# Optimization experiments

Measured on AMD Instinct MI355X. Metric: run time of the kernel, lower is better.

Reference implementation:

```python
import jax, jax.numpy as jnp
import numpy as np

N_NODES = 50000
N_EDGES = 800000
IN_DIM = 128
HID = 128
BN_EPS = 1e-5


def setup_inputs() -> dict:
    key = jax.random.key(0)
    ks = jax.random.split(key, 8)
    x = jax.random.normal(ks[0], (N_NODES, IN_DIM), dtype=jnp.float32)
    edge_index = jax.random.randint(ks[1], (2, N_EDGES), 0, N_NODES, dtype=jnp.int64)
    s1 = 1.0 / np.sqrt(IN_DIM)
    s2 = 1.0 / np.sqrt(HID)
    return {
        'x': x,
        'edge_index': edge_index,
        'w1_0': jax.random.normal(ks[2], (IN_DIM, HID), dtype=jnp.float32) * s1,
        'b1_0': jnp.zeros((HID,), dtype=jnp.float32),
        'w2_0': jax.random.normal(ks[3], (HID, HID), dtype=jnp.float32) * s2,
        'b2_0': jnp.zeros((HID,), dtype=jnp.float32),
        'g_0': jnp.ones((HID,), dtype=jnp.float32),
        'be_0': jnp.zeros((HID,), dtype=jnp.float32),
        'w1_1': jax.random.normal(ks[4], (HID, HID), dtype=jnp.float32) * s2,
        'b1_1': jnp.zeros((HID,), dtype=jnp.float32),
        'w2_1': jax.random.normal(ks[5], (HID, HID), dtype=jnp.float32) * s2,
        'b2_1': jnp.zeros((HID,), dtype=jnp.float32),
        'g_1': jnp.ones((HID,), dtype=jnp.float32),
        'be_1': jnp.zeros((HID,), dtype=jnp.float32),
    }


def _gin_layer(h, src, dst, w1, b1, w2, b2, g, be):
    # GINConv with eps=0: MLP(h_i + sum_{j->i} h_j); scatter-add over targets
    agg = jax.ops.segment_sum(h[src], dst, num_segments=N_NODES)
    z = h + agg
    z = jax.nn.relu(z @ w1 + b1) @ w2 + b2
    # BatchNorm1d (training mode: batch stats over nodes, biased variance)
    mu = jnp.mean(z, axis=0)
    var = jnp.mean(jnp.square(z - mu), axis=0)
    z = (z - mu) * jax.lax.rsqrt(var + BN_EPS) * g + be
    return jax.nn.relu(z)


def reference(x, edge_index, w1_0, b1_0, w2_0, b2_0, g_0, be_0,
              w1_1, b1_1, w2_1, b2_1, g_1, be_1):
    src, dst = edge_index[0], edge_index[1]
    h = _gin_layer(x, src, dst, w1_0, b1_0, w2_0, b2_0, g_0, be_0)
    # dropout p=0.0 -> no-op between layers
    h = _gin_layer(h, src, dst, w1_1, b1_1, w2_1, b2_1, g_1, be_1)
    return h
```

## Files before the change

kernel.cpp:

```cpp
#include <hip/hip_runtime.h>
#include <hip/hip_bf16.h>

#define HID 128
#define LDA 136
#define BINSH 4
#define BINSZ 16
#define NBH 3136
#define EPB 4096
#define ECAP 768
#define CAP 64

typedef __attribute__((ext_vector_type(8))) short frag8;
typedef __attribute__((ext_vector_type(4))) float f32x4;

__device__ inline float bf2f(unsigned short u) {
    return __uint_as_float(((unsigned int)u) << 16);
}
__device__ inline unsigned short f2bf(float f) {
    __hip_bfloat16 h = __float2bfloat16(f);
    return __builtin_bit_cast(unsigned short, h);
}
__device__ inline float4 u4tof4(ushort4 u) {
    return make_float4(bf2f(u.x), bf2f(u.y), bf2f(u.z), bf2f(u.w));
}
__device__ inline ushort4 f4tou4(float4 f) {
    ushort4 u; u.x = f2bf(f.x); u.y = f2bf(f.y); u.z = f2bf(f.z); u.w = f2bf(f.w);
    return u;
}
__device__ inline void unpack8(uint4 u, float* f) {
    const unsigned* w = (const unsigned*)&u;
    #pragma unroll
    for (int j = 0; j < 4; j++) {
        f[2 * j]     = __uint_as_float(w[j] << 16);
        f[2 * j + 1] = __uint_as_float(w[j] & 0xffff0000u);
    }
}

__global__ __launch_bounds__(256) void hist_k(
    const int* __restrict__ dst, int* __restrict__ Hst,
    const float* __restrict__ x, unsigned short* __restrict__ B0,
    const float* __restrict__ w0, const float* __restrict__ w1,
    const float* __restrict__ w2, const float* __restrict__ w3,
    unsigned short* __restrict__ wt,
    int n_edges, long total4, int hb, int vb)
{
    __shared__ int hist[NBH];
    const int bid = blockIdx.x;
    const int t = threadIdx.x;

    if (bid < hb) {
        for (int j = t; j < NBH; j += 256) hist[j] = 0;
        __syncthreads();
        const int base = bid * EPB;
        const int cnt = min(EPB, n_edges - base);
        for (int i = t; i < cnt; i += 256)
            atomicAdd(&hist[dst[base + i] >> BINSH], 1);
        __syncthreads();
        for (int j = t; j < NBH; j += 256)
            Hst[(size_t)bid * NBH + j] = hist[j];
    } else if (bid < hb + vb) {
        long i = (long)(bid - hb) * 256 + t;
        if (i < total4) {
            float4 v = ((const float4*)x)[i];
            ((ushort4*)B0)[i] = f4tou4(v);
        }
    } else {
        int w_id = bid - hb - vb;
        const float* w = (w_id == 0) ? w0 : (w_id == 1) ? w1 : (w_id == 2) ? w2 : w3;
        unsigned short* o = wt + (size_t)w_id * 128 * 128;
        for (int i = 0; i < 64; i++) {
            int idx = t + i * 256;
            o[(idx & 127) * 128 + (idx >> 7)] = f2bf(w[idx]);
        }
    }
}

__global__ __launch_bounds__(256) void colscan_k(
    int* __restrict__ Hst, int* __restrict__ colsum, int nblk)
{
    int b = blockIdx.x * 256 + threadIdx.x;
    if (b >= NBH) return;
    int run = 0;
    int i = 0;
    for (; i + 4 <= nblk; i += 4) {
        int* p0 = &Hst[(size_t)(i + 0) * NBH + b];
        int* p1 = &Hst[(size_t)(i + 1) * NBH + b];
        int* p2 = &Hst[(size_t)(i + 2) * NBH + b];
        int* p3 = &Hst[(size_t)(i + 3) * NBH + b];
        int v0 = *p0, v1 = *p1, v2 = *p2, v3 = *p3;
        *p0 = run; run += v0;
        *p1 = run; run += v1;
        *p2 = run; run += v2;
        *p3 = run; run += v3;
    }
    for (; i < nblk; i++) {
        int v = Hst[(size_t)i * NBH + b];
        Hst[(size_t)i * NBH + b] = run;
        run += v;
    }
    colsum[b] = run;
}

__global__ __launch_bounds__(1024) void binscan_k(
    const int* __restrict__ colsum, int* __restrict__ binStart,
    float* __restrict__ S0, float* __restrict__ S1)
{
    __shared__ int s[NBH];
    __shared__ int c[1024];
    const int t = threadIdx.x;
    if (t < 256) S0[t] = 0.f;
    else if (t < 512) S1[t - 256] = 0.f;
    for (int j = t; j < NBH; j += 1024) s[j] = colsum[j];
    __syncthreads();

    int l0 = 0, l1 = 0, l2 = 0, l3 = 0, sum = 0;
    if (t < NBH / 4) {
        int b = t * 4;
        l0 = s[b]; l1 = s[b + 1]; l2 = s[b + 2]; l3 = s[b + 3];
        sum = l0 + l1 + l2 + l3;
    }
    c[t] = sum;
    __syncthreads();
    for (int off = 1; off < 1024; off <<= 1) {
        int v = (t >= off) ? c[t - off] : 0;
        __syncthreads();
        c[t] += v;
        __syncthreads();
    }
    if (t < NBH / 4) {
        int ex = c[t] - sum;
        int b = t * 4;
        binStart[b] = ex;
        binStart[b + 1] = ex + l0;
        binStart[b + 2] = ex + l0 + l1;
        binStart[b + 3] = ex + l0 + l1 + l2;
    }
}

__global__ __launch_bounds__(256) void place_k(
    const int* __restrict__ src, const int* __restrict__ dst,
    const int* __restrict__ Hst, const int* __restrict__ binStart,
    int* __restrict__ binned, int n_edges)
{
    __shared__ int hist[NBH];
    const int bid = blockIdx.x;
    const int t = threadIdx.x;
    for (int j = t; j < NBH; j += 256) hist[j] = 0;
    __syncthreads();
    const int base = bid * EPB;
    const int cnt = min(EPB, n_edges - base);
    const int* Hrow = Hst + (size_t)bid * NBH;
    for (int i = t; i < cnt; i += 256) {
        int e = base + i;
        int d = dst[e];
        int bin = d >> BINSH;
        int r = atomicAdd(&hist[bin], 1);
        int pos = binStart[bin] + Hrow[bin] + r;
        binned[pos] = (src[e] << BINSH) | (d & (BINSZ - 1));
    }
}

template<bool BN>
__global__ __launch_bounds__(512) void gather_k(
    const unsigned short* __restrict__ h, unsigned short* __restrict__ z,
    const int* __restrict__ binStart, const int* __restrict__ colsum,
    const int* __restrict__ binned,
    const float* __restrict__ S, const float* __restrict__ g,
    const float* __restrict__ be, float inv_n, int n)
{
    __shared__ int Ls[ECAP];
    __shared__ int cnt16[BINSZ];
    __shared__ int perNode[BINSZ * CAP];
    __shared__ float lscS[BN ? 128 : 1], lshS[BN ? 128 : 1];

    const int t = threadIdx.x;
    const int bin = blockIdx.x;
    const int v0 = bin << BINSH;

    if (t < BINSZ) cnt16[t] = 0;
    if (BN && t < 128) {
        float mu = S[t] * inv_n;
        float var = fmaf(-mu, mu, S[128 + t] * inv_n);
        float s = g[t] * rsqrtf(var + 1e-5f);
        lscS[t] = s;
        lshS[t] = fmaf(-mu, s, be[t]);
    }
    const int base = binStart[bin];
    const int total = min(colsum[bin], ECAP);
    for (int j = t; j < total; j += 512) Ls[j] = binned[base + j];
    __syncthreads();

    for (int j = t; j < total; j += 512) {
        int pa = Ls[j];
        int node = pa & (BINSZ - 1);
        int p = atomicAdd(&cnt16[node], 1);
        if (p < CAP) perNode[node * CAP + p] = pa >> BINSH;
    }
    __syncthreads();

    const int vl = t >> 5;
    const int v = v0 + vl;
    if (v >= n) return;
    const int lane = t & 31;
    const int fs = (lane & 15) * 8;
    const int par = lane >> 4;

    float sc[8], sh[8];
    if (BN) {
        #pragma unroll
        for (int j = 0; j < 8; j++) { sc[j] = lscS[fs + j]; sh[j] = lshS[fs + j]; }
    }

    float acc[8];
    #pragma unroll
    for (int j = 0; j < 8; j++) acc[j] = 0.f;

    if (par == 0) {
        uint4 u = *(const uint4*)(h + (size_t)v * HID + fs);
        float f[8];
        unpack8(u, f);
        #pragma unroll
        for (int j = 0; j < 8; j++) {
            float xv = f[j];
            if (BN) xv = fmaxf(fmaf(xv, sc[j], sh[j]), 0.f);
            acc[j] = xv;
        }
    }

    const int* bucket = perNode + vl * CAP;
    int deg = min(cnt16[vl], CAP);

    int i = par;
    for (; i + 6 < deg; i += 8) {
        int s0 = bucket[i], s1 = bucket[i + 2];
        int s2 = bucket[i + 4], s3 = bucket[i + 6];
        uint4 u0 = *(const uint4*)(h + (size_t)s0 * HID + fs);
        uint4 u1 = *(const uint4*)(h + (size_t)s1 * HID + fs);
        uint4 u2 = *(const uint4*)(h + (size_t)s2 * HID + fs);
        uint4 u3 = *(const uint4*)(h + (size_t)s3 * HID + fs);
        float f0[8], f1[8], f2[8], f3[8];
        unpack8(u0, f0); unpack8(u1, f1); unpack8(u2, f2); unpack8(u3, f3);
        if (BN) {
            #pragma unroll
            for (int j = 0; j < 8; j++) {
                f0[j] = fmaxf(fmaf(f0[j], sc[j], sh[j]), 0.f);
                f1[j] = fmaxf(fmaf(f1[j], sc[j], sh[j]), 0.f);
                f2[j] = fmaxf(fmaf(f2[j], sc[j], sh[j]), 0.f);
                f3[j] = fmaxf(fmaf(f3[j], sc[j], sh[j]), 0.f);
            }
        }
        #pragma unroll
        for (int j = 0; j < 8; j++)
            acc[j] += (f0[j] + f1[j]) + (f2[j] + f3[j]);
    }
    for (; i < deg; i += 2) {
        uint4 u = *(const uint4*)(h + (size_t)bucket[i] * HID + fs);
        float f[8];
        unpack8(u, f);
        if (BN) {
            #pragma unroll
            for (int j = 0; j < 8; j++)
                f[j] = fmaxf(fmaf(f[j], sc[j], sh[j]), 0.f);
        }
        #pragma unroll
        for (int j = 0; j < 8; j++) acc[j] += f[j];
    }

    #pragma unroll
    for (int j = 0; j < 8; j++) acc[j] += __shfl_xor(acc[j], 16);

    if (par == 0) {
        unsigned o[4];
        #pragma unroll
        for (int j = 0; j < 4; j++)
            o[j] = (unsigned)f2bf(acc[2 * j]) |
                   ((unsigned)f2bf(acc[2 * j + 1]) << 16);
        *(uint4*)(z + (size_t)v * HID + fs) = make_uint4(o[0], o[1], o[2], o[3]);
    }
}

__global__ __launch_bounds__(256) void mlp_k(
    unsigned short* __restrict__ Z,
    const unsigned short* __restrict__ W1t, const float* __restrict__ b1,
    const unsigned short* __restrict__ W2t, const float* __restrict__ b2,
    float* __restrict__ S, int n_rows)
{
    __shared__ unsigned short Hs[128 * LDA];
    __shared__ float red[1024];

    const int t = threadIdx.x;
    const int row0 = blockIdx.x * 128;
    const int wave = t >> 6;
    const int lane = t & 63;
    const int l15  = lane & 15;
    const int quad = lane >> 4;

    const int r0 = row0 + wave * 32 + l15;
    const int r1 = r0 + 16;
    const int rs0 = (r0 < n_rows) ? r0 : 0;
    const int rs1 = (r1 < n_rows) ? r1 : 0;
    frag8 a0[4], a1[4];
    #pragma unroll
    for (int kk = 0; kk < 4; kk++) {
        a0[kk] = *(const frag8*)(Z + (size_t)rs0 * HID + kk * 32 + quad * 8);
        a1[kk] = *(const frag8*)(Z + (size_t)rs1 * HID + kk * 32 + quad * 8);
    }

    f32x4 acc[2][8];
    #pragma unroll
    for (int tr = 0; tr < 2; tr++)
        #pragma unroll
        for (int tc = 0; tc < 8; tc++)
            acc[tr][tc] = (f32x4){0.f, 0.f, 0.f, 0.f};

    #pragma unroll
    for (int kk = 0; kk < 4; kk++) {
        int ko = kk * 32 + quad * 8;
        #pragma unroll
        for (int tc = 0; tc < 8; tc++) {
            frag8 b = *(const frag8*)(W1t + (size_t)(tc * 16 + l15) * HID + ko);
            acc[0][tc] = __builtin_amdgcn_mfma_f32_16x16x32_bf16(a0[kk], b, acc[0][tc], 0, 0, 0);
            acc[1][tc] = __builtin_amdgcn_mfma_f32_16x16x32_bf16(a1[kk], b, acc[1][tc], 0, 0, 0);
        }
    }

    const int wrow = wave * 32;
    #pragma unroll
    for (int tc = 0; tc < 8; tc++) {
        const int col = tc * 16 + l15;
        const float bc = b1[col];
        #pragma unroll
        for (int tr = 0; tr < 2; tr++)
            #pragma unroll
            for (int r = 0; r < 4; r++) {
                int lrow = wrow + tr * 16 + quad * 4 + r;
                Hs[lrow * LDA + col] = f2bf(fmaxf(acc[tr][tc][r] + bc, 0.f));
            }
    }
    __syncthreads();

    #pragma unroll
    for (int kk = 0; kk < 4; kk++) {
        a0[kk] = *(const frag8*)(Hs + (wave * 32 + l15) * LDA + kk * 32 + quad * 8);
        a1[kk] = *(const frag8*)(Hs + (wave * 32 + 16 + l15) * LDA + kk * 32 + quad * 8);
    }
    #pragma unroll
    for (int tr = 0; tr < 2; tr++)
        #pragma unroll
        for (int tc = 0; tc < 8; tc++)
            acc[tr][tc] = (f32x4){0.f, 0.f, 0.f, 0.f};

    #pragma unroll
    for (int kk = 0; kk < 4; kk++) {
        int ko = kk * 32 + quad * 8;
        #pragma unroll
        for (int tc = 0; tc < 8; tc++) {
            frag8 b = *(const frag8*)(W2t + (size_t)(tc * 16 + l15) * HID + ko);
            acc[0][tc] = __builtin_amdgcn_mfma_f32_16x16x32_bf16(a0[kk], b, acc[0][tc], 0, 0, 0);
            acc[1][tc] = __builtin_amdgcn_mfma_f32_16x16x32_bf16(a1[kk], b, acc[1][tc], 0, 0, 0);
        }
    }

    #pragma unroll
    for (int tc = 0; tc < 8; tc++) {
        const int col = tc * 16 + l15;
        const float bc = b2[col];
        float s = 0.f, sq = 0.f;
        #pragma unroll
        for (int tr = 0; tr < 2; tr++)
            #pragma unroll
            for (int r = 0; r < 4; r++) {
                int grow = row0 + wrow + tr * 16 + quad * 4 + r;
                float o = acc[tr][tc][r] + bc;
                if (grow < n_rows) {
                    s += o; sq = fmaf(o, o, sq);
                    Z[(size_t)grow * HID + col] = f2bf(o);
                }
            }
        s  += __shfl_xor(s, 16);  s  += __shfl_xor(s, 32);
        sq += __shfl_xor(sq, 16); sq += __shfl_xor(sq, 32);
        if (lane < 16) {
            red[wave * 128 + col] = s;
            red[512 + wave * 128 + col] = sq;
        }
    }
    __syncthreads();
    {
        int which = t >> 7, c = t & 127;
        const float* rp = red + which * 512;
        atomicAdd(&S[which * 128 + c],
                  rp[c] + rp[128 + c] + rp[256 + c] + rp[384 + c]);
    }
}

__global__ __launch_bounds__(256) void bn_apply_f32_k(
    const unsigned short* __restrict__ z, const float* __restrict__ S,
    const float* __restrict__ g, const float* __restrict__ be,
    float* __restrict__ out, float inv_n, long total4)
{
    __shared__ float lsc[128], lsh[128];
    int t = threadIdx.x;
    if (t < 128) {
        float mu = S[t] * inv_n;
        float var = fmaf(-mu, mu, S[128 + t] * inv_n);
        float s = g[t] * rsqrtf(var + 1e-5f);
        lsc[t] = s;
        lsh[t] = fmaf(-mu, s, be[t]);
    }
    __syncthreads();

    long i = blockIdx.x * 256L + t;
    if (i >= total4) return;
    float4 v = u4tof4(((const ushort4*)z)[i]);
    int c0 = ((int)(i & 31)) * 4;
    v.x = fmaxf(fmaf(v.x, lsc[c0 + 0], lsh[c0 + 0]), 0.0f);
    v.y = fmaxf(fmaf(v.y, lsc[c0 + 1], lsh[c0 + 1]), 0.0f);
    v.z = fmaxf(fmaf(v.z, lsc[c0 + 2], lsh[c0 + 2]), 0.0f);
    v.w = fmaxf(fmaf(v.w, lsc[c0 + 3], lsh[c0 + 3]), 0.0f);
    ((float4*)out)[i] = v;
}

extern "C" void kernel_launch(void* const* d_in, const int* in_sizes, int n_in,
                              void* d_out, int out_size, void* d_ws, size_t ws_size,
                              hipStream_t stream)
{
    const float* x    = (const float*)d_in[0];
    const int*   ei   = (const int*)d_in[1];
    const float* w1_0 = (const float*)d_in[2];
    const float* b1_0 = (const float*)d_in[3];
    const float* w2_0 = (const float*)d_in[4];
    const float* b2_0 = (const float*)d_in[5];
    const float* g_0  = (const float*)d_in[6];
    const float* be_0 = (const float*)d_in[7];
    const float* w1_1 = (const float*)d_in[8];
    const float* b1_1 = (const float*)d_in[9];
    const float* w2_1 = (const float*)d_in[10];
    const float* b2_1 = (const float*)d_in[11];
    const float* g_1  = (const float*)d_in[12];
    const float* be_1 = (const float*)d_in[13];
    float* OUT = (float*)d_out;

    const int n       = in_sizes[0] / HID;
    const int n_edges = in_sizes[1] / 2;
    const int* src = ei;
    const int* dst = ei + n_edges;
    const float inv_n = 1.0f / (float)n;
    const int n_bins = (n + BINSZ - 1) / BINSZ;

    char* p = (char*)d_ws;
    unsigned short* B0 = (unsigned short*)p;  p += (size_t)n * HID * sizeof(short);
    unsigned short* B1 = (unsigned short*)p;  p += (size_t)n * HID * sizeof(short);
    unsigned short* Wt = (unsigned short*)p;  p += (size_t)4 * 128 * 128 * sizeof(short);
    const int nblk = (n_edges + EPB - 1) / EPB;
    int*   Hst      = (int*)p;   p += (size_t)nblk * NBH * sizeof(int);
    int*   colsum   = (int*)p;   p += NBH * sizeof(int);
    int*   binStart = (int*)p;   p += NBH * sizeof(int);
    float* S0       = (float*)p; p += 256 * sizeof(float);
    float* S1       = (float*)p; p += 256 * sizeof(float);
    int*   binned   = (int*)p;   p += (size_t)n_edges * sizeof(int);

    dim3 blk(256);
    const long total4 = (long)n * (HID / 4);
    const int vb = (int)((total4 + 255) / 256);

    hist_k<<<nblk + vb + 4, blk, 0, stream>>>(
        dst, Hst, x, B0, w1_0, w2_0, w1_1, w2_1, Wt, n_edges, total4, nblk, vb);
    colscan_k<<<(NBH + 255) / 256, blk, 0, stream>>>(Hst, colsum, nblk);
    binscan_k<<<1, dim3(1024), 0, stream>>>(colsum, binStart, S0, S1);
    place_k<<<nblk, blk, 0, stream>>>(src, dst, Hst, binStart, binned, n_edges);

    gather_k<false><<<n_bins, dim3(512), 0, stream>>>(
        B0, B1, binStart, colsum, binned, nullptr, nullptr, nullptr, inv_n, n);
    mlp_k<<<(n + 127) / 128, blk, 0, stream>>>(B1, Wt, b1_0, Wt + 16384, b2_0, S0, n);

    gather_k<true><<<n_bins, dim3(512), 0, stream>>>(
        B1, B0, binStart, colsum, binned, S0, g_0, be_0, inv_n, n);
    mlp_k<<<(n + 127) / 128, blk, 0, stream>>>(B0, Wt + 2 * 16384, b1_1,
                                               Wt + 3 * 16384, b2_1, S1, n);
    bn_apply_f32_k<<<vb, blk, 0, stream>>>(B0, S1, g_1, be_1, OUT, inv_n, total4);
}
```

Before: 282.5 us.

## Fuse neighbor gather into MLP kernel with 128-node bins and separate BN pass

```diff
diff --git a/kernel.cpp b/kernel.cpp
--- a/kernel.cpp
+++ b/kernel.cpp
@@ -7,7 +7,6 @@
 #define BINSZ 16
 #define NBH 3136
 #define EPB 4096
-#define ECAP 768
 #define CAP 64
 
 typedef __attribute__((ext_vector_type(8))) short frag8;
@@ -156,171 +155,119 @@
         int bin = d >> BINSH;
         int r = atomicAdd(&hist[bin], 1);
         int pos = binStart[bin] + Hrow[bin] + r;
-        binned[pos] = (src[e] << BINSH) | (d & (BINSZ - 1));
-    }
-}
-
-template<bool BN>
-__global__ __launch_bounds__(512) void gather_k(
-    const unsigned short* __restrict__ h, unsigned short* __restrict__ z,
-    const int* __restrict__ binStart, const int* __restrict__ colsum,
-    const int* __restrict__ binned,
-    const float* __restrict__ S, const float* __restrict__ g,
-    const float* __restrict__ be, float inv_n, int n)
-{
-    __shared__ int Ls[ECAP];
-    __shared__ int cnt16[BINSZ];
-    __shared__ int perNode[BINSZ * CAP];
-    __shared__ float lscS[BN ? 128 : 1], lshS[BN ? 128 : 1];
+        binned[pos] = (src[e] << 7) | (d & 127);
+    }
+}
+
+__device__ inline void gather_row(const unsigned short* __restrict__ Hin,
+                                  int gr, int n, const int* __restrict__ bp,
+                                  int deg, int fo, frag8* out)
+{
+    float acc[4][8];
+    if (gr < n) {
+        #pragma unroll
+        for (int kk = 0; kk < 4; kk++) {
+            uint4 u = *(const uint4*)(Hin + (size_t)gr * HID + fo + kk * 32);
+            unpack8(u, acc[kk]);
+        }
+    } else {
+        #pragma unroll
+        for (int kk = 0; kk < 4; kk++)
+            #pragma unroll
+            for (int j = 0; j < 8; j++) acc[kk][j] = 0.f;
+    }
+    int i = 0;
+    for (; i + 2 <= deg; i += 2) {
+        int sA = bp[i], sB = bp[i + 1];
+        uint4 uA[4], uB[4];
+        #pragma unroll
+        for (int kk = 0; kk < 4; kk++) {
+            uA[kk] = *(const uint4*)(Hin + (size_t)sA * HID + fo + kk * 32);
+            uB[kk] = *(const uint4*)(Hin + (size_t)sB * HID + fo + kk * 32);
+        }
+        #pragma unroll
+        for (int kk = 0; kk < 4; kk++) {
+            float fA[8], fB[8];
+            unpack8(uA[kk], fA);
+            unpack8(uB[kk], fB);
+            #pragma unroll
+            for (int j = 0; j < 8; j++) acc[kk][j] += fA[j] + fB[j];
+        }
+    }
+    if (i < deg) {
+        int sA = bp[i];
+        #pragma unroll
+        for (int kk = 0; kk < 4; kk++) {
+            uint4 u = *(const uint4*)(Hin + (size_t)sA * HID + fo + kk * 32);
+            float fA[8];
+            unpack8(u, fA);
+            #pragma unroll
+            for (int j = 0; j < 8; j++) acc[kk][j] += fA[j];
+        }
+    }
+    #pragma unroll
+    for (int kk = 0; kk < 4; kk++) {
+        frag8 f;
+        #pragma unroll
+        for (int j = 0; j < 8; j++) f[j] = (short)f2bf(acc[kk][j]);
+        out[kk] = f;
+    }
+}
+
+__global__ __launch_bounds__(256) void gmlp_k(
+    const unsigned short* __restrict__ Hin, unsigned short* __restrict__ Zout,
+    const int* __restrict__ binStart, const int* __restrict__ binned,
+    const float* __restrict__ b1v, const unsigned short* __restrict__ W1t,
+    const float* __restrict__ b2v, const unsigned short* __restrict__ W2t,
+    float* __restrict__ SOut, int n, int n_edges)
+{
+    __shared__ __align__(16) unsigned char uS[128 * LDA * 2];
+    int* perNode = (int*)uS;
+    unsigned short* Hs = (unsigned short*)uS;
+    __shared__ int cnt[128];
+    __shared__ float red[1024];
 
     const int t = threadIdx.x;
-    const int bin = blockIdx.x;
-    const int v0 = bin << BINSH;
-
-    if (t < BINSZ) cnt16[t] = 0;
-    if (BN && t < 128) {
-        float mu = S[t] * inv_n;
-        float var = fmaf(-mu, mu, S[128 + t] * inv_n);
-        float s = g[t] * rsqrtf(var + 1e-5f);
-        lscS[t] = s;
-        lshS[t] = fmaf(-mu, s, be[t]);
-    }
-    const int base = binStart[bin];
-    const int total = min(colsum[bin], ECAP);
-    for (int j = t; j < total; j += 512) Ls[j] = binned[base + j];
-    __syncthreads();
-
-    for (int j = t; j < total; j += 512) {
-        int pa = Ls[j];
-        int node = pa & (BINSZ - 1);
-        int p = atomicAdd(&cnt16[node], 1);
-        if (p < CAP) perNode[node * CAP + p] = pa >> BINSH;
-    }
-    __syncthreads();
-
-    const int vl = t >> 5;
-    const int v = v0 + vl;
-    if (v >= n) return;
-    const int lane = t & 31;
-    const int fs = (lane & 15) * 8;
-    const int par = lane >> 4;
-
-    float sc[8], sh[8];
-    if (BN) {
-        #pragma unroll
-        for (int j = 0; j < 8; j++) { sc[j] = lscS[fs + j]; sh[j] = lshS[fs + j]; }
-    }
-
-    float acc[8];
-    #pragma unroll
-    for (int j = 0; j < 8; j++) acc[j] = 0.f;
-
-    if (par == 0) {
-        uint4 u = *(const uint4*)(h + (size_t)v * HID + fs);
-        float f[8];
-        unpack8(u, f);
-        #pragma unroll
-        for (int j = 0; j < 8; j++) {
-            float xv = f[j];
-            if (BN) xv = fmaxf(fmaf(xv, sc[j], sh[j]), 0.f);
-            acc[j] = xv;
-        }
-    }
-
-    const int* bucket = perNode + vl * CAP;
-    int deg = min(cnt16[vl], CAP);
-
-    int i = par;
-    for (; i + 6 < deg; i += 8) {
-        int s0 = bucket[i], s1 = bucket[i + 2];
-        int s2 = bucket[i + 4], s3 = bucket[i + 6];
-        uint4 u0 = *(const uint4*)(h + (size_t)s0 * HID + fs);
-        uint4 u1 = *(const uint4*)(h + (size_t)s1 * HID + fs);
-        uint4 u2 = *(const uint4*)(h + (size_t)s2 * HID + fs);
-        uint4 u3 = *(const uint4*)(h + (size_t)s3 * HID + fs);
-        float f0[8], f1[8], f2[8], f3[8];
-        unpack8(u0, f0); unpack8(u1, f1); unpack8(u2, f2); unpack8(u3, f3);
-        if (BN) {
-            #pragma unroll
-            for (int j = 0; j < 8; j++) {
-                f0[j] = fmaxf(fmaf(f0[j], sc[j], sh[j]), 0.f);
-                f1[j] = fmaxf(fmaf(f1[j], sc[j], sh[j]), 0.f);
-                f2[j] = fmaxf(fmaf(f2[j], sc[j], sh[j]), 0.f);
-                f3[j] = fmaxf(fmaf(f3[j], sc[j], sh[j]), 0.f);
-            }
-        }
-        #pragma unroll
-        for (int j = 0; j < 8; j++)
-            acc[j] += (f0[j] + f1[j]) + (f2[j] + f3[j]);
-    }
-    for (; i < deg; i += 2) {
-        uint4 u = *(const uint4*)(h + (size_t)bucket[i] * HID + fs);
-        float f[8];
-        unpack8(u, f);
-        if (BN) {
-            #pragma unroll
-            for (int j = 0; j < 8; j++)
-                f[j] = fmaxf(fmaf(f[j], sc[j], sh[j]), 0.f);
-        }
-        #pragma unroll
-        for (int j = 0; j < 8; j++) acc[j] += f[j];
-    }
-
-    #pragma unroll
-    for (int j = 0; j < 8; j++) acc[j] += __shfl_xor(acc[j], 16);
-
-    if (par == 0) {
-        unsigned o[4];
-        #pragma unroll
-        for (int j = 0; j < 4; j++)
-            o[j] = (unsigned)f2bf(acc[2 * j]) |
-                   ((unsigned)f2bf(acc[2 * j + 1]) << 16);
-        *(uint4*)(z + (size_t)v * HID + fs) = make_uint4(o[0], o[1], o[2], o[3]);
-    }
-}
-
-__global__ __launch_bounds__(256) void mlp_k(
-    unsigned short* __restrict__ Z,
-    const unsigned short* __restrict__ W1t, const float* __restrict__ b1,
-    const unsigned short* __restrict__ W2t, const float* __restrict__ b2,
-    float* __restrict__ S, int n_rows)
-{
-    __shared__ unsigned short Hs[128 * LDA];
-    __shared__ float red[1024];
-
-    const int t = threadIdx.x;
-    const int row0 = blockIdx.x * 128;
-    const int wave = t >> 6;
-    const int lane = t & 63;
-    const int l15  = lane & 15;
-    const int quad = lane >> 4;
-
-    const int r0 = row0 + wave * 32 + l15;
-    const int r1 = r0 + 16;
-    const int rs0 = (r0 < n_rows) ? r0 : 0;
-    const int rs1 = (r1 < n_rows) ? r1 : 0;
+    const int v0 = blockIdx.x * 128;
+
+    if (t < 128) cnt[t] = 0;
+    __syncthreads();
+
+    const int gbin = blockIdx.x * 8;
+    const int jstart = binStart[gbin];
+    const int jend = binStart[gbin + 8];
+    for (int j = jstart + t; j < jend; j += 256) {
+        int e = binned[j];
+        int node = e & 127;
+        int p = atomicAdd(&cnt[node], 1);
+        if (p < CAP) perNode[node * CAP + p] = e >> 7;
+    }
+    __syncthreads();
+
+    const int wave = t >> 6, lane = t & 63, l15 = lane & 15, quad = lane >> 4;
+    const int lr0 = wave * 32 + l15, lr1 = lr0 + 16;
+    const int fo = quad * 8;
+
     frag8 a0[4], a1[4];
+    gather_row(Hin, v0 + lr0, n, perNode + lr0 * CAP, min(cnt[lr0], CAP), fo, a0);
+    gather_row(Hin, v0 + lr1, n, perNode + lr1 * CAP, min(cnt[lr1], CAP), fo, a1);
+    __syncthreads();
+
+    f32x4 macc[2][8];
+    #pragma unroll
+    for (int tr = 0; tr < 2; tr++)
+        #pragma unroll
+        for (int tc = 0; tc < 8; tc++)
+            macc[tr][tc] = (f32x4){0.f, 0.f, 0.f, 0.f};
+
     #pragma unroll
     for (int kk = 0; kk < 4; kk++) {
-        a0[kk] = *(const frag8*)(Z + (size_t)rs0 * HID + kk * 32 + quad * 8);
-        a1[kk] = *(const frag8*)(Z + (size_t)rs1 * HID + kk * 32 + quad * 8);
-    }
-
-    f32x4 acc[2][8];
-    #pragma unroll
-    for (int tr = 0; tr < 2; tr++)
-        #pragma unroll
-        for (int tc = 0; tc < 8; tc++)
-            acc[tr][tc] = (f32x4){0.f, 0.f, 0.f, 0.f};
-
-    #pragma unroll
-    for (int kk = 0; kk < 4; kk++) {
-        int ko = kk * 32 + quad * 8;
+        int ko = fo + kk * 32;
         #pragma unroll
         for (int tc = 0; tc < 8; tc++) {
             frag8 b = *(const frag8*)(W1t + (size_t)(tc * 16 + l15) * HID + ko);
-            acc[0][tc] = __builtin_amdgcn_mfma_f32_16x16x32_bf16(a0[kk], b, acc[0][tc], 0, 0, 0);
-            acc[1][tc] = __builtin_amdgcn_mfma_f32_16x16x32_bf16(a1[kk], b, acc[1][tc], 0, 0, 0);
+            macc[0][tc] = __builtin_amdgcn_mfma_f32_16x16x32_bf16(a0[kk], b, macc[0][tc], 0, 0, 0);
+            macc[1][tc] = __builtin_amdgcn_mfma_f32_16x16x32_bf16(a1[kk], b, macc[1][tc], 0, 0, 0);
         }
     }
 
@@ -328,53 +275,53 @@
     #pragma unroll
     for (int tc = 0; tc < 8; tc++) {
         const int col = tc * 16 + l15;
-        const float bc = b1[col];
+        const float bc = b1v[col];
         #pragma unroll
         for (int tr = 0; tr < 2; tr++)
             #pragma unroll
             for (int r = 0; r < 4; r++) {
                 int lrow = wrow + tr * 16 + quad * 4 + r;
-                Hs[lrow * LDA + col] = f2bf(fmaxf(acc[tr][tc][r] + bc, 0.f));
+                Hs[lrow * LDA + col] = f2bf(fmaxf(macc[tr][tc][r] + bc, 0.f));
             }
     }
     __syncthreads();
 
     #pragma unroll
     for (int kk = 0; kk < 4; kk++) {
-        a0[kk] = *(const frag8*)(Hs + (wave * 32 + l15) * LDA + kk * 32 + quad * 8);
-        a1[kk] = *(const frag8*)(Hs + (wave * 32 + 16 + l15) * LDA + kk * 32 + quad * 8);
+        a0[kk] = *(const frag8*)(Hs + (wrow + l15) * LDA + fo + kk * 32);
+        a1[kk] = *(const frag8*)(Hs + (wrow + 16 + l15) * LDA + fo + kk * 32);
     }
     #pragma unroll
     for (int tr = 0; tr < 2; tr++)
         #pragma unroll
         for (int tc = 0; tc < 8; tc++)
-            acc[tr][tc] = (f32x4){0.f, 0.f, 0.f, 0.f};
+            macc[tr][tc] = (f32x4){0.f, 0.f, 0.f, 0.f};
 
     #pragma unroll
     for (int kk = 0; kk < 4; kk++) {
-        int ko = kk * 32 + quad * 8;
+        int ko = fo + kk * 32;
         #pragma unroll
         for (int tc = 0; tc < 8; tc++) {
             frag8 b = *(const frag8*)(W2t + (size_t)(tc * 16 + l15) * HID + ko);
-            acc[0][tc] = __builtin_amdgcn_mfma_f32_16x16x32_bf16(a0[kk], b, acc[0][tc], 0, 0, 0);
-            acc[1][tc] = __builtin_amdgcn_mfma_f32_16x16x32_bf16(a1[kk], b, acc[1][tc], 0, 0, 0);
+            macc[0][tc] = __builtin_amdgcn_mfma_f32_16x16x32_bf16(a0[kk], b, macc[0][tc], 0, 0, 0);
+            macc[1][tc] = __builtin_amdgcn_mfma_f32_16x16x32_bf16(a1[kk], b, macc[1][tc], 0, 0, 0);
         }
     }
 
     #pragma unroll
     for (int tc = 0; tc < 8; tc++) {
         const int col = tc * 16 + l15;
-        const float bc = b2[col];
+        const float bc = b2v[col];
         float s = 0.f, sq = 0.f;
         #pragma unroll
         for (int tr = 0; tr < 2; tr++)
             #pragma unroll
             for (int r = 0; r < 4; r++) {
-                int grow = row0 + wrow + tr * 16 + quad * 4 + r;
-                float o = acc[tr][tc][r] + bc;
-                if (grow < n_rows) {
+                int grow = v0 + wrow + tr * 16 + quad * 4 + r;
+                float o = macc[tr][tc][r] + bc;
+                if (grow < n) {
                     s += o; sq = fmaf(o, o, sq);
-                    Z[(size_t)grow * HID + col] = f2bf(o);
+                    Zout[(size_t)grow * HID + col] = f2bf(o);
                 }
             }
         s  += __shfl_xor(s, 16);  s  += __shfl_xor(s, 32);
@@ -388,9 +335,36 @@
     {
         int which = t >> 7, c = t & 127;
         const float* rp = red + which * 512;
-        atomicAdd(&S[which * 128 + c],
+        atomicAdd(&SOut[which * 128 + c],
                   rp[c] + rp[128 + c] + rp[256 + c] + rp[384 + c]);
     }
+}
+
+__global__ __launch_bounds__(256) void bnmat_k(
+    const unsigned short* __restrict__ z, const float* __restrict__ S,
+    const float* __restrict__ g, const float* __restrict__ be,
+    unsigned short* __restrict__ out, float inv_n, long total4)
+{
+    __shared__ float lsc[128], lsh[128];
+    int t = threadIdx.x;
+    if (t < 128) {
+        float mu = S[t] * inv_n;
+        float var = fmaf(-mu, mu, S[128 + t] * inv_n);
+        float s = g[t] * rsqrtf(var + 1e-5f);
+        lsc[t] = s;
+        lsh[t] = fmaf(-mu, s, be[t]);
+    }
+    __syncthreads();
+
+    long i = blockIdx.x * 256L + t;
+    if (i >= total4) return;
+    float4 v = u4tof4(((const ushort4*)z)[i]);
+    int c0 = ((int)(i & 31)) * 4;
+    v.x = fmaxf(fmaf(v.x, lsc[c0 + 0], lsh[c0 + 0]), 0.0f);
+    v.y = fmaxf(fmaf(v.y, lsc[c0 + 1], lsh[c0 + 1]), 0.0f);
+    v.z = fmaxf(fmaf(v.z, lsc[c0 + 2], lsh[c0 + 2]), 0.0f);
+    v.w = fmaxf(fmaf(v.w, lsc[c0 + 3], lsh[c0 + 3]), 0.0f);
+    ((ushort4*)out)[i] = f4tou4(v);
 }
 
 __global__ __launch_bounds__(256) void bn_apply_f32_k(
@@ -445,7 +419,6 @@
     const int* src = ei;
     const int* dst = ei + n_edges;
     const float inv_n = 1.0f / (float)n;
-    const int n_bins = (n + BINSZ - 1) / BINSZ;
 
     char* p = (char*)d_ws;
     unsigned short* B0 = (unsigned short*)p;  p += (size_t)n * HID * sizeof(short);
@@ -459,9 +432,12 @@
     float* S1       = (float*)p; p += 256 * sizeof(float);
     int*   binned   = (int*)p;   p += (size_t)n_edges * sizeof(int);
 
+    unsigned short* B2 = (unsigned short*)d_out;
+
     dim3 blk(256);
     const long total4 = (long)n * (HID / 4);
     const int vb = (int)((total4 + 255) / 256);
+    const int gmlp_blocks = (n + 127) / 128;
 
     hist_k<<<nblk + vb + 4, blk, 0, stream>>>(
         dst, Hst, x, B0, w1_0, w2_0, w1_1, w2_1, Wt, n_edges, total4, nblk, vb);
@@ -469,13 +445,12 @@
     binscan_k<<<1, dim3(1024), 0, stream>>>(colsum, binStart, S0, S1);
     place_k<<<nblk, blk, 0, stream>>>(src, dst, Hst, binStart, binned, n_edges);
 
-    gather_k<false><<<n_bins, dim3(512), 0, stream>>>(
-        B0, B1, binStart, colsum, binned, nullptr, nullptr, nullptr, inv_n, n);
-    mlp_k<<<(n + 127) / 128, blk, 0, stream>>>(B1, Wt, b1_0, Wt + 16384, b2_0, S0, n);
-
-    gather_k<true><<<n_bins, dim3(512), 0, stream>>>(
-        B1, B0, binStart, colsum, binned, S0, g_0, be_0, inv_n, n);
-    mlp_k<<<(n + 127) / 128, blk, 0, stream>>>(B0, Wt + 2 * 16384, b1_1,
-                                               Wt + 3 * 16384, b2_1, S1, n);
+    gmlp_k<<<gmlp_blocks, blk, 0, stream>>>(
+        B0, B1, binStart, binned, b1_0, Wt, b2_0, Wt + 16384, S0, n, n_edges);
+
+    bnmat_k<<<vb, blk, 0, stream>>>(B1, S0, g_0, be_0, B2, inv_n, total4);
+    gmlp_k<<<gmlp_blocks, blk, 0, stream>>>(
+        B2, B0, binStart, binned, b1_1, Wt + 2 * 16384, b2_1, Wt + 3 * 16384,
+        S1, n, n_edges);
     bn_apply_f32_k<<<vb, blk, 0, stream>>>(B0, S1, g_1, be_1, OUT, inv_n, total4);
 }
```

New measurement: 304.0 us. 7.6% more time.
